# Performance work log

Measured on AMD Instinct MI355X. Metric: run time of the kernel, lower is better.

Reference implementation:

```python
import jax, jax.numpy as jnp
import numpy as np

D_MODEL = 1024
EXPANDED = 1024  # d_model * expansion_factor(1.0)
K = 3
EPS = 1e-8


def rms_norm(x, w, eps=EPS):
    return x * jax.lax.rsqrt(jnp.mean(x * x, axis=-1, keepdims=True) + eps) * w


def setup_inputs() -> dict:
    key = jax.random.key(0)
    ks = jax.random.split(key, 8)
    b, t = 4, 4096
    u = jax.random.normal(ks[0], (b, t, D_MODEL), dtype=jnp.float32)
    s_in = 1.0 / np.sqrt(D_MODEL)
    s_out = 1.0 / np.sqrt(EXPANDED)
    W_in = jax.random.uniform(ks[1], (2 * EXPANDED, D_MODEL), jnp.float32, -s_in, s_in)
    b_in = jax.random.uniform(ks[2], (2 * EXPANDED,), jnp.float32, -s_in, s_in)
    in_norm_w = jnp.ones((2 * EXPANDED,), jnp.float32)
    s_conv = 1.0 / np.sqrt(K)  # groups=expanded_dim -> fan_in = K
    conv_w = jax.random.uniform(ks[3], (EXPANDED, 1, K), jnp.float32, -s_conv, s_conv)
    conv_b = jax.random.uniform(ks[4], (EXPANDED,), jnp.float32, -s_conv, s_conv)
    W_out = jax.random.uniform(ks[5], (D_MODEL, EXPANDED), jnp.float32, -s_out, s_out)
    b_out = jax.random.uniform(ks[6], (D_MODEL,), jnp.float32, -s_out, s_out)
    out_norm_w = jnp.ones((D_MODEL,), jnp.float32)
    return {
        "u": u, "W_in": W_in, "b_in": b_in, "in_norm_w": in_norm_w,
        "conv_w": conv_w, "conv_b": conv_b,
        "W_out": W_out, "b_out": b_out, "out_norm_w": out_norm_w,
    }


def reference(u, W_in, b_in, in_norm_w, conv_w, conv_b, W_out, b_out, out_norm_w):
    # in_proj + RMSNorm
    xv = rms_norm(jnp.einsum('btd,ed->bte', u, W_in) + b_in, in_norm_w)  # [b,t,2E]
    x, v = jnp.split(xv, 2, axis=-1)  # each [b,t,E]
    # depthwise 'same' conv along time: NCH layout
    x_f = jnp.transpose(x, (0, 2, 1))  # [b,E,t]
    pad = (K - 1) // 2
    y = jax.lax.conv_general_dilated(
        x_f, conv_w, window_strides=(1,), padding=[(pad, pad)],
        dimension_numbers=('NCH', 'OIH', 'NCH'), feature_group_count=EXPANDED)
    y = y + conv_b[None, :, None]
    x_mixed = jnp.transpose(y, (0, 2, 1))  # [b,t,E]
    gated = v * x_mixed
    out = rms_norm(jnp.einsum('bte,de->btd', gated, W_out) + b_out, out_norm_w)
    return out
```

## Files before the change

### kernel.cpp

```cpp
#include <hip/hip_runtime.h>

#define BT    16384
#define TSEQ  4096
#define DM    1024
#define EXP   1024
#define N1    2048
#define KDIM  1024
#define EPSV  1e-8f

typedef __bf16 bf16x8 __attribute__((ext_vector_type(8)));
typedef float f32x16 __attribute__((ext_vector_type(16)));
typedef unsigned short u16x8 __attribute__((ext_vector_type(8)));

#define AS1CAST(p) ((__attribute__((address_space(1))) void*)(p))
#define AS3CAST(p) ((__attribute__((address_space(3))) void*)(p))

__device__ __forceinline__ unsigned short f2bf(float f) {
    unsigned int u = __float_as_uint(f);
    u += 0x7fffu + ((u >> 16) & 1u);
    return (unsigned short)(u >> 16);
}

__global__ __launch_bounds__(256) void k_f2bf3(const float* __restrict__ i0, unsigned short* __restrict__ o0, int n0,
                                               const float* __restrict__ i1, unsigned short* __restrict__ o1, int n1,
                                               const float* __restrict__ i2, unsigned short* __restrict__ o2, int n2) {
    int i = blockIdx.x * 256 + threadIdx.x;
    const float* in; unsigned short* out;
    if (i < n0)                { in = i0; out = o0; }
    else if (i < n0 + n1)      { in = i1; out = o1; i -= n0; }
    else if (i < n0 + n1 + n2) { in = i2; out = o2; i -= n0 + n1; }
    else return;
    float4 v = ((const float4*)in)[i];
    ushort4 o;
    o.x = f2bf(v.x); o.y = f2bf(v.y); o.z = f2bf(v.z); o.w = f2bf(v.w);
    ((ushort4*)out)[i] = o;
}

template <int BF16_OUT>
__device__ __forceinline__ void gemm_body(const unsigned short* __restrict__ A,
                                          const unsigned short* __restrict__ Bw,
                                          const float* __restrict__ bias,
                                          unsigned short* __restrict__ Cb,
                                          float* __restrict__ Cf,
                                          float* __restrict__ ssq,
                                          int N) {
    __shared__ unsigned short sA[128 * 64];
    __shared__ unsigned short sB[128 * 64];

    const int tid  = threadIdx.x;
    const int lane = tid & 63;
    const int wv   = tid >> 6;
    const int wm   = wv >> 1, wn = wv & 1;
    const int row0 = blockIdx.y * 128, col0 = blockIdx.x * 128;

    const int p7 = tid & 7;
    const unsigned short* aPtr[4];
    const unsigned short* bPtr[4];
#pragma unroll
    for (int b = 0; b < 4; ++b) {
        const int r = (b * 256 + tid) >> 3;
        const int q = (p7 - r) & 7;
        aPtr[b] = A  + (size_t)(row0 + r) * KDIM + q * 8;
        bPtr[b] = Bw + (size_t)(col0 + r) * KDIM + q * 8;
    }
    unsigned short* lA[4];
    unsigned short* lB[4];
#pragma unroll
    for (int b = 0; b < 4; ++b) {
        lA[b] = sA + (b * 256 + wv * 64) * 8;
        lB[b] = sB + (b * 256 + wv * 64) * 8;
    }

    const int ln = lane & 31;
    const int hi = lane >> 5;
    const int arow0 = (wm * 64 + ln) * 64;
    const int brow0 = (wn * 64 + ln) * 64;

    f32x16 acc[2][2] = {};

    for (int kt = 0; kt < KDIM / 64; ++kt) {
        __syncthreads();
#pragma unroll
        for (int b = 0; b < 4; ++b) {
            __builtin_amdgcn_global_load_lds(AS1CAST(aPtr[b] + kt * 64), AS3CAST(lA[b]), 16, 0, 0);
            __builtin_amdgcn_global_load_lds(AS1CAST(bPtr[b] + kt * 64), AS3CAST(lB[b]), 16, 0, 0);
        }
        __syncthreads();

#pragma unroll
        for (int ks = 0; ks < 4; ++ks) {
            const int sw = (((ks * 2 + hi) + ln) & 7) * 8;
            bf16x8 aF[2], bF[2];
#pragma unroll
            for (int i = 0; i < 2; ++i) {
                aF[i] = *(const bf16x8*)&sA[arow0 + i * 32 * 64 + sw];
                bF[i] = *(const bf16x8*)&sB[brow0 + i * 32 * 64 + sw];
            }
#pragma unroll
            for (int i = 0; i < 2; ++i)
#pragma unroll
                for (int j = 0; j < 2; ++j)
                    acc[i][j] = __builtin_amdgcn_mfma_f32_32x32x16_bf16(
                        aF[i], bF[j], acc[i][j], 0, 0, 0);
        }
    }

    const int c0 = col0 + wn * 64 + ln;
    const float bs0 = bias[c0], bs1 = bias[c0 + 32];

#pragma unroll
    for (int i = 0; i < 2; ++i) {
        const int rbase = row0 + wm * 64 + i * 32 + 4 * hi;
#pragma unroll
        for (int reg = 0; reg < 16; ++reg) {
            const int gm = rbase + (reg & 3) + 8 * (reg >> 2);
            float v0 = acc[i][0][reg] + bs0;
            float v1 = acc[i][1][reg] + bs1;
            float p = v0 * v0 + v1 * v1;
#pragma unroll
            for (int off = 1; off < 32; off <<= 1) p += __shfl_xor(p, off, 64);
            if (ln == 0) atomicAdd(&ssq[gm], p);
            size_t base = (size_t)gm * N + c0;
            if (BF16_OUT) {
                Cb[base]      = f2bf(v0);
                Cb[base + 32] = f2bf(v1);
            } else {
                Cf[base]      = v0;
                Cf[base + 32] = v1;
            }
        }
    }
}

__global__ __launch_bounds__(256) void k_gemm_in(const unsigned short* __restrict__ A,
                                                 const unsigned short* __restrict__ Bw,
                                                 const float* __restrict__ bias,
                                                 unsigned short* __restrict__ Cb,
                                                 float* __restrict__ ssq) {
    gemm_body<1>(A, Bw, bias, Cb, nullptr, ssq, N1);
}

__global__ __launch_bounds__(256) void k_gemm_out(const unsigned short* __restrict__ A,
                                                  const unsigned short* __restrict__ Bw,
                                                  const float* __restrict__ bias,
                                                  float* __restrict__ Cf,
                                                  float* __restrict__ ssq) {
    gemm_body<0>(A, Bw, bias, nullptr, Cf, ssq, DM);
}

__global__ __launch_bounds__(256) void k_conv_gate(const unsigned short* __restrict__ z,
                                                   const float* __restrict__ ssq1,
                                                   const float* __restrict__ inw,
                                                   const float* __restrict__ cw,
                                                   const float* __restrict__ cb,
                                                   unsigned short* __restrict__ g) {
    const int tok = blockIdx.x * 2 + (threadIdx.x >> 7);
    const int e8  = (threadIdx.x & 127) * 8;
    const int t   = tok & (TSEQ - 1);

    const float rs0 = rsqrtf(ssq1[tok] * (1.0f / N1) + EPSV);
    const int tm = (t > 0) ? tok - 1 : tok;
    const int tp = (t < TSEQ - 1) ? tok + 1 : tok;
    const float rsm = (t > 0) ? rsqrtf(ssq1[tm] * (1.0f / N1) + EPSV) : 0.0f;
    const float rsp = (t < TSEQ - 1) ? rsqrtf(ssq1[tp] * (1.0f / N1) + EPSV) : 0.0f;

    bf16x8 xm = *(const bf16x8*)(z + (size_t)tm * N1 + e8);
    bf16x8 x0 = *(const bf16x8*)(z + (size_t)tok * N1 + e8);
    bf16x8 xp = *(const bf16x8*)(z + (size_t)tp * N1 + e8);
    bf16x8 vv = *(const bf16x8*)(z + (size_t)tok * N1 + EXP + e8);

    u16x8 ov;
#pragma unroll
    for (int p = 0; p < 8; ++p) {
        const int e = e8 + p;
        const float we  = inw[e];
        const float wvv = inw[EXP + e];
        const float w0 = cw[e * 3], w1 = cw[e * 3 + 1], w2 = cw[e * 3 + 2];
        float y = w0 * ((float)xm[p] * rsm * we)
                + w1 * ((float)x0[p] * rs0 * we)
                + w2 * ((float)xp[p] * rsp * we)
                + cb[e];
        float vn = (float)vv[p] * rs0 * wvv;
        ov[p] = f2bf(vn * y);
    }
    *(u16x8*)(g + (size_t)tok * EXP + e8) = ov;
}

__global__ __launch_bounds__(256) void k_outnorm(float* __restrict__ o,
                                                 const float* __restrict__ ssq2,
                                                 const float* __restrict__ onw) {
    const int idx = blockIdx.x * 256 + threadIdx.x;
    const int tok = idx >> 8;
    const int d4  = (idx & 255) * 4;
    const float rs = rsqrtf(ssq2[tok] * (1.0f / DM) + EPSV);
    float4 v = ((float4*)o)[idx];
    float4 w = *(const float4*)(onw + d4);
    v.x *= rs * w.x; v.y *= rs * w.y; v.z *= rs * w.z; v.w *= rs * w.w;
    ((float4*)o)[idx] = v;
}

extern "C" void kernel_launch(void* const* d_in, const int* in_sizes, int n_in,
                              void* d_out, int out_size, void* d_ws, size_t ws_size,
                              hipStream_t stream) {
    const float* u     = (const float*)d_in[0];
    const float* W_in  = (const float*)d_in[1];
    const float* b_in  = (const float*)d_in[2];
    const float* inw   = (const float*)d_in[3];
    const float* cw    = (const float*)d_in[4];
    const float* cb    = (const float*)d_in[5];
    const float* W_out = (const float*)d_in[6];
    const float* b_out = (const float*)d_in[7];
    const float* onw   = (const float*)d_in[8];
    float* out = (float*)d_out;

    char* ws = (char*)d_ws;
    unsigned short* u_bf    = (unsigned short*)ws; ws += (size_t)BT * DM * 2;
    unsigned short* Win_bf  = (unsigned short*)ws; ws += (size_t)N1 * DM * 2;
    unsigned short* Wout_bf = (unsigned short*)ws; ws += (size_t)DM * EXP * 2;
    unsigned short* z_bf    = (unsigned short*)ws; ws += (size_t)BT * N1 * 2;
    unsigned short* g_bf    = (unsigned short*)ws; ws += (size_t)BT * EXP * 2;
    float* ssq1 = (float*)ws; ws += (size_t)BT * 4;
    float* ssq2 = (float*)ws; ws += (size_t)BT * 4;

    hipMemsetAsync(ssq1, 0, (size_t)BT * 2 * sizeof(float), stream);

    const int n0 = BT * DM / 4, n1c = N1 * DM / 4, n2c = DM * EXP / 4;
    k_f2bf3<<<(n0 + n1c + n2c + 255) / 256, 256, 0, stream>>>(u, u_bf, n0,
                                                              W_in, Win_bf, n1c,
                                                              W_out, Wout_bf, n2c);

    dim3 gA(N1 / 128, BT / 128);
    k_gemm_in<<<gA, 256, 0, stream>>>(u_bf, Win_bf, b_in, z_bf, ssq1);

    k_conv_gate<<<BT / 2, 256, 0, stream>>>(z_bf, ssq1, inw, cw, cb, g_bf);

    dim3 gC(DM / 128, BT / 128);
    k_gemm_out<<<gC, 256, 0, stream>>>(g_bf, Wout_bf, b_out, out, ssq2);

    k_outnorm<<<BT, 256, 0, stream>>>(out, ssq2, onw);

    (void)in_sizes; (void)n_in; (void)out_size; (void)ws_size;
}
```

Baseline: 324.2 us.

## Load A fragments directly to registers and stage only B in LDS

The GEMM now uses 2 waves (128 threads) per 128x128 tile. Each wave computes 64 rows by 128 columns. A fragments are loaded straight from global memory into registers and double-buffered one K-step ahead, while only the B tile is staged in LDS via global_load_lds. This halves LDS traffic and footprint and doubles MFMA work per B fragment read, at the cost of more registers per thread and uncoalesced per-lane global loads for A. The intent is to cut LDS bandwidth and overlap A fetches with compute.

```diff
diff --git a/kernel.cpp b/kernel.cpp
--- a/kernel.cpp
+++ b/kernel.cpp
@@ -6,6 +6,7 @@
 #define EXP   1024
 #define N1    2048
 #define KDIM  1024
+#define NKT   (KDIM / 64)
 #define EPSV  1e-8f
 
 typedef __bf16 bf16x8 __attribute__((ext_vector_type(8)));
@@ -44,107 +45,112 @@
                                           float* __restrict__ Cf,
                                           float* __restrict__ ssq,
                                           int N) {
-    __shared__ unsigned short sA[128 * 64];
     __shared__ unsigned short sB[128 * 64];
 
     const int tid  = threadIdx.x;
     const int lane = tid & 63;
-    const int wv   = tid >> 6;
-    const int wm   = wv >> 1, wn = wv & 1;
+    const int w    = tid >> 6;
+    const int ln   = lane & 31;
+    const int hi   = lane >> 5;
     const int row0 = blockIdx.y * 128, col0 = blockIdx.x * 128;
 
-    const int p7 = tid & 7;
-    const unsigned short* aPtr[4];
-    const unsigned short* bPtr[4];
-#pragma unroll
-    for (int b = 0; b < 4; ++b) {
-        const int r = (b * 256 + tid) >> 3;
-        const int q = (p7 - r) & 7;
-        aPtr[b] = A  + (size_t)(row0 + r) * KDIM + q * 8;
-        bPtr[b] = Bw + (size_t)(col0 + r) * KDIM + q * 8;
+    const unsigned short* aRow0 = A + (size_t)(row0 + w * 64 + ln) * KDIM + hi * 8;
+    const unsigned short* aRow1 = aRow0 + (size_t)32 * KDIM;
+
+    const int r_b = tid >> 3;
+    const int q_b = ((tid & 7) - r_b) & 7;
+    const unsigned short* bSrc = Bw + (size_t)(col0 + r_b) * KDIM + q_b * 8;
+
+    f32x16 acc[2][4] = {};
+
+    auto loadA = [&](bf16x8* ar, int kt) {
+#pragma unroll
+        for (int ks = 0; ks < 4; ++ks) {
+            ar[ks]     = *(const bf16x8*)(aRow0 + kt * 64 + ks * 16);
+            ar[4 + ks] = *(const bf16x8*)(aRow1 + kt * 64 + ks * 16);
+        }
+    };
+    auto stageB = [&](int kt) {
+#pragma unroll
+        for (int b = 0; b < 8; ++b)
+            __builtin_amdgcn_global_load_lds(AS1CAST(bSrc + (size_t)b * 16 * KDIM + kt * 64),
+                                             AS3CAST(&sB[(b * 128 + w * 64) * 8]), 16, 0, 0);
+    };
+    auto compute = [&](const bf16x8* ar) {
+#pragma unroll
+        for (int ks = 0; ks < 4; ++ks) {
+            const int sw = ((ks * 2 + hi + ln) & 7) * 8;
+            bf16x8 bF[4];
+#pragma unroll
+            for (int j = 0; j < 4; ++j)
+                bF[j] = *(const bf16x8*)&sB[(j * 32 + ln) * 64 + sw];
+#pragma unroll
+            for (int i = 0; i < 2; ++i)
+#pragma unroll
+                for (int j = 0; j < 4; ++j)
+                    acc[i][j] = __builtin_amdgcn_mfma_f32_32x32x16_bf16(
+                        ar[i * 4 + ks], bF[j], acc[i][j], 0, 0, 0);
+        }
+    };
+
+    bf16x8 a0[8], a1[8];
+    loadA(a0, 0);
+    for (int kt = 0; kt < NKT; kt += 2) {
+        __syncthreads();
+        stageB(kt);
+        loadA(a1, kt + 1);
+        __syncthreads();
+        compute(a0);
+        __syncthreads();
+        stageB(kt + 1);
+        if (kt + 2 < NKT) loadA(a0, kt + 2);
+        __syncthreads();
+        compute(a1);
     }
-    unsigned short* lA[4];
-    unsigned short* lB[4];
-#pragma unroll
-    for (int b = 0; b < 4; ++b) {
-        lA[b] = sA + (b * 256 + wv * 64) * 8;
-        lB[b] = sB + (b * 256 + wv * 64) * 8;
-    }
-
-    const int ln = lane & 31;
-    const int hi = lane >> 5;
-    const int arow0 = (wm * 64 + ln) * 64;
-    const int brow0 = (wn * 64 + ln) * 64;
-
-    f32x16 acc[2][2] = {};
-
-    for (int kt = 0; kt < KDIM / 64; ++kt) {
-        __syncthreads();
-#pragma unroll
-        for (int b = 0; b < 4; ++b) {
-            __builtin_amdgcn_global_load_lds(AS1CAST(aPtr[b] + kt * 64), AS3CAST(lA[b]), 16, 0, 0);
-            __builtin_amdgcn_global_load_lds(AS1CAST(bPtr[b] + kt * 64), AS3CAST(lB[b]), 16, 0, 0);
-        }
-        __syncthreads();
-
-#pragma unroll
-        for (int ks = 0; ks < 4; ++ks) {
-            const int sw = (((ks * 2 + hi) + ln) & 7) * 8;
-            bf16x8 aF[2], bF[2];
-#pragma unroll
-            for (int i = 0; i < 2; ++i) {
-                aF[i] = *(const bf16x8*)&sA[arow0 + i * 32 * 64 + sw];
-                bF[i] = *(const bf16x8*)&sB[brow0 + i * 32 * 64 + sw];
+
+    const int c0 = col0 + ln;
+    float bs[4];
+#pragma unroll
+    for (int j = 0; j < 4; ++j) bs[j] = bias[c0 + j * 32];
+
+#pragma unroll
+    for (int i = 0; i < 2; ++i) {
+        const int rb = row0 + w * 64 + i * 32 + 4 * hi;
+#pragma unroll
+        for (int reg = 0; reg < 16; ++reg) {
+            const int gm = rb + (reg & 3) + 8 * (reg >> 2);
+            float v[4]; float p = 0.f;
+#pragma unroll
+            for (int j = 0; j < 4; ++j) {
+                v[j] = acc[i][j][reg] + bs[j];
+                p += v[j] * v[j];
             }
-#pragma unroll
-            for (int i = 0; i < 2; ++i)
-#pragma unroll
-                for (int j = 0; j < 2; ++j)
-                    acc[i][j] = __builtin_amdgcn_mfma_f32_32x32x16_bf16(
-                        aF[i], bF[j], acc[i][j], 0, 0, 0);
-        }
-    }
-
-    const int c0 = col0 + wn * 64 + ln;
-    const float bs0 = bias[c0], bs1 = bias[c0 + 32];
-
-#pragma unroll
-    for (int i = 0; i < 2; ++i) {
-        const int rbase = row0 + wm * 64 + i * 32 + 4 * hi;
-#pragma unroll
-        for (int reg = 0; reg < 16; ++reg) {
-            const int gm = rbase + (reg & 3) + 8 * (reg >> 2);
-            float v0 = acc[i][0][reg] + bs0;
-            float v1 = acc[i][1][reg] + bs1;
-            float p = v0 * v0 + v1 * v1;
 #pragma unroll
             for (int off = 1; off < 32; off <<= 1) p += __shfl_xor(p, off, 64);
             if (ln == 0) atomicAdd(&ssq[gm], p);
             size_t base = (size_t)gm * N + c0;
-            if (BF16_OUT) {
-                Cb[base]      = f2bf(v0);
-                Cb[base + 32] = f2bf(v1);
-            } else {
-                Cf[base]      = v0;
-                Cf[base + 32] = v1;
+#pragma unroll
+            for (int j = 0; j < 4; ++j) {
+                if (BF16_OUT) Cb[base + j * 32] = f2bf(v[j]);
+                else          Cf[base + j * 32] = v[j];
             }
         }
     }
 }
 
-__global__ __launch_bounds__(256) void k_gemm_in(const unsigned short* __restrict__ A,
-                                                 const unsigned short* __restrict__ Bw,
-                                                 const float* __restrict__ bias,
-                                                 unsigned short* __restrict__ Cb,
-                                                 float* __restrict__ ssq) {
+__global__ __launch_bounds__(128, 2) void k_gemm_in(const unsigned short* __restrict__ A,
+                                                    const unsigned short* __restrict__ Bw,
+                                                    const float* __restrict__ bias,
+                                                    unsigned short* __restrict__ Cb,
+                                                    float* __restrict__ ssq) {
     gemm_body<1>(A, Bw, bias, Cb, nullptr, ssq, N1);
 }
 
-__global__ __launch_bounds__(256) void k_gemm_out(const unsigned short* __restrict__ A,
-                                                  const unsigned short* __restrict__ Bw,
-                                                  const float* __restrict__ bias,
-                                                  float* __restrict__ Cf,
-                                                  float* __restrict__ ssq) {
+__global__ __launch_bounds__(128, 2) void k_gemm_out(const unsigned short* __restrict__ A,
+                                                     const unsigned short* __restrict__ Bw,
+                                                     const float* __restrict__ bias,
+                                                     float* __restrict__ Cf,
+                                                     float* __restrict__ ssq) {
     gemm_body<0>(A, Bw, bias, nullptr, Cf, ssq, DM);
 }
 
@@ -230,12 +236,12 @@
                                                               W_out, Wout_bf, n2c);
 
     dim3 gA(N1 / 128, BT / 128);
-    k_gemm_in<<<gA, 256, 0, stream>>>(u_bf, Win_bf, b_in, z_bf, ssq1);
+    k_gemm_in<<<gA, 128, 0, stream>>>(u_bf, Win_bf, b_in, z_bf, ssq1);
 
     k_conv_gate<<<BT / 2, 256, 0, stream>>>(z_bf, ssq1, inw, cw, cb, g_bf);
 
     dim3 gC(DM / 128, BT / 128);
-    k_gemm_out<<<gC, 256, 0, stream>>>(g_bf, Wout_bf, b_out, out, ssq2);
+    k_gemm_out<<<gC, 128, 0, stream>>>(g_bf, Wout_bf, b_out, out, ssq2);
 
     k_outnorm<<<BT, 256, 0, stream>>>(out, ssq2, onw);
 
```

Measured after the change: 346.1 us. 6.8% more time.
